# Kernel optimization log

Hardware: AMD Instinct MI355X
Metric: run time of the kernel (lower is better)

## Reference

```python
import jax, jax.numpy as jnp
import numpy as np

B, T_PAST, FUTURE_N = 128, 1024, 512
IN_F, IP, H, OUT_F = 64, 128, 256, 64


def _init(key, shape, fan_in):
    return (jax.random.uniform(key, shape, jnp.float32) * 2.0 - 1.0) / np.sqrt(fan_in).astype(np.float32)


def setup_inputs() -> dict:
    key = jax.random.key(0)
    ks = jax.random.split(key, 16)
    return {
        "x": jax.random.normal(ks[0], (B, T_PAST, IN_F), jnp.float32),
        "future_n": FUTURE_N,
        # encoder: Linear(IN_F -> IP)
        "enc_W": _init(ks[1], (IP, IN_F), IN_F),
        "enc_b": _init(ks[2], (IP,), IN_F),
        # future encoder: Linear(H -> IP)
        "fut_W": _init(ks[3], (IP, H), H),
        "fut_b": _init(ks[4], (IP,), H),
        # decoder: Linear(H -> OUT_F)
        "dec_W": _init(ks[5], (OUT_F, H), H),
        "dec_b": _init(ks[6], (OUT_F,), H),
        # past LSTMCell(IP, H)
        "pW_ih": _init(ks[7], (4 * H, IP), H),
        "pW_hh": _init(ks[8], (4 * H, H), H),
        "pb_ih": _init(ks[9], (4 * H,), H),
        "pb_hh": _init(ks[10], (4 * H,), H),
        # future LSTMCell(IP, H)
        "fW_ih": _init(ks[11], (4 * H, IP), H),
        "fW_hh": _init(ks[12], (4 * H, H), H),
        "fb_ih": _init(ks[13], (4 * H,), H),
        "fb_hh": _init(ks[14], (4 * H,), H),
    }


def _lstm_cell(xt, h, c, W_ih, W_hh, b_ih, b_hh):
    # torch LSTMCell gate order: i, f, g, o
    gates = xt @ W_ih.T + h @ W_hh.T + (b_ih + b_hh)
    i, f, g, o = jnp.split(gates, 4, axis=-1)
    c_new = jax.nn.sigmoid(f) * c + jax.nn.sigmoid(i) * jnp.tanh(g)
    h_new = jax.nn.sigmoid(o) * jnp.tanh(c_new)
    return h_new, c_new


def reference(x, future_n, enc_W, enc_b, fut_W, fut_b, dec_W, dec_b,
              pW_ih, pW_hh, pb_ih, pb_hh, fW_ih, fW_hh, fb_ih, fb_hh):
    batch = x.shape[0]
    hidden = pW_hh.shape[1]
    h0 = jnp.zeros((batch, hidden), x.dtype)
    c0 = jnp.zeros((batch, hidden), x.dtype)

    encoded = x @ enc_W.T + enc_b  # [B, T, IP]

    def past_step(carry, xt):
        h, c = carry
        h, c = _lstm_cell(xt, h, c, pW_ih, pW_hh, pb_ih, pb_hh)
        return (h, c), h

    (h, c), hs_past = jax.lax.scan(past_step, (h0, c0), jnp.swapaxes(encoded, 0, 1))

    def fut_step(carry, _):
        h, c = carry
        inp = h @ fut_W.T + fut_b
        h, c = _lstm_cell(inp, h, c, fW_ih, fW_hh, fb_ih, fb_hh)
        return (h, c), h

    _, hs_fut = jax.lax.scan(fut_step, (h, c), None, length=future_n)

    hs = jnp.concatenate([hs_past, hs_fut], axis=0)  # [T+F, B, H]
    out = jnp.swapaxes(hs, 0, 1) @ dec_W.T + dec_b  # [B, T+F, OUT_F]
    return out
```

## Files before the change

kernel.cpp:

```cpp
#include <hip/hip_runtime.h>

#define B_    128
#define TPAST 1024
#define FN    512
#define TT    1536
#define INF   64
#define IPF   128
#define HD    256
#define NG    1024
#define OUTF  64

typedef _Float16 f16;
typedef _Float16 f16x8 __attribute__((ext_vector_type(8)));
typedef _Float16 f16x4 __attribute__((ext_vector_type(4)));
typedef float    f32x4 __attribute__((ext_vector_type(4)));

template<int N> struct ic { static constexpr int value = N; };

__device__ __forceinline__ float sigm_(float x) {
  return __builtin_amdgcn_rcpf(1.f + __expf(-x));
}
__device__ __forceinline__ float tanh_(float x) {
  return 1.f - 2.f * __builtin_amdgcn_rcpf(1.f + __expf(2.f * x));
}
__device__ __forceinline__ f16x8 oload16(const f16* p) {
  f16x8 v;
  asm volatile("global_load_dwordx4 %0, %1, off\n\ts_waitcnt vmcnt(0)"
               : "=v"(v) : "v"(p));
  return v;
}

extern "C" __global__ void eprep(
    const float* __restrict__ enc_W, const float* __restrict__ enc_b,
    const float* __restrict__ fut_W, const float* __restrict__ fut_b,
    const float* __restrict__ dec_W,
    const float* __restrict__ pW_ih, const float* __restrict__ pW_hh,
    const float* __restrict__ pb_ih, const float* __restrict__ pb_hh,
    const float* __restrict__ fW_ih, const float* __restrict__ fW_hh,
    const float* __restrict__ fb_ih, const float* __restrict__ fb_hh,
    f16* __restrict__ Wp_in, float* __restrict__ bp,
    f16* __restrict__ Wp16, f16* __restrict__ Wf16,
    float* __restrict__ bf, f16* __restrict__ dW16)
{
  int stride = gridDim.x * blockDim.x;
  int gid = blockIdx.x * blockDim.x + threadIdx.x;
  for (int i = gid; i < NG * HD; i += stride) {
    int n = i >> 8, j = i & 255;
    float s = fW_hh[i];
    for (int m = 0; m < IPF; ++m) s += fW_ih[n * IPF + m] * fut_W[m * HD + j];
    Wf16[i] = (f16)s;
    Wp16[i] = (f16)pW_hh[i];
  }
  for (int i = gid; i < NG * INF; i += stride) {
    int n = i >> 6, k = i & 63;
    float s = 0.f;
    for (int m = 0; m < IPF; ++m) s += pW_ih[n * IPF + m] * enc_W[m * INF + k];
    Wp_in[i] = (f16)s;
  }
  for (int i = gid; i < OUTF * HD; i += stride) dW16[i] = (f16)dec_W[i];
  for (int n = gid; n < NG; n += stride) {
    float s1 = pb_ih[n] + pb_hh[n], s2 = fb_ih[n] + fb_hh[n];
    for (int m = 0; m < IPF; ++m) {
      s1 += pW_ih[n * IPF + m] * enc_b[m];
      s2 += fW_ih[n * IPF + m] * fut_b[m];
    }
    bp[n] = s1; bf[n] = s2;
  }
}

extern "C" __global__ __launch_bounds__(64) void epgemm(
    const float* __restrict__ x, const f16* __restrict__ Wp_in,
    const float* __restrict__ bp, f16* __restrict__ P, int t0, int Tc)
{
  int wg = blockIdx.x;
  int tl = wg >> 3, bt = wg & 7;
  int t = t0 + tl;
  int l = (int)threadIdx.x, r = l & 15, g = l >> 4;
  const float* xb = x + ((size_t)(bt * 16 + r) * TPAST + t) * INF;
  f16x8 a[2];
#pragma unroll
  for (int kk = 0; kk < 2; ++kk) {
    const float* px = xb + kk * 32 + g * 8;
    f32x4 v0 = *(const f32x4*)px;
    f32x4 v1 = *(const f32x4*)(px + 4);
#pragma unroll
    for (int e = 0; e < 4; ++e) { a[kk][e] = (f16)v0[e]; a[kk][4 + e] = (f16)v1[e]; }
  }
  for (int nt = 0; nt < 64; ++nt) {
    int n = nt * 16 + r;
    f16x8 b0 = *(const f16x8*)(Wp_in + (size_t)n * INF + g * 8);
    f16x8 b1 = *(const f16x8*)(Wp_in + (size_t)n * INF + 32 + g * 8);
    f32x4 acc = {0.f, 0.f, 0.f, 0.f};
    acc = __builtin_amdgcn_mfma_f32_16x16x32_f16(a[0], b0, acc, 0, 0, 0);
    acc = __builtin_amdgcn_mfma_f32_16x16x32_f16(a[1], b1, acc, 0, 0, 0);
    float bias = bp[n];
    f16x4 hv;
#pragma unroll
    for (int e = 0; e < 4; ++e) hv[e] = (f16)(acc[e] + bias);
    int jh = (n >> 7) & 1;
    int nl = (n >> 8) * 128 + (n & 127);
    f16* Pt = P + (((size_t)(jh * 8 + bt) * Tc + tl) * 512 + nl) * 16;
    *(f16x4*)(Pt + 4 * g) = hv;
  }
}

extern "C" __global__ __launch_bounds__(256, 1)
void erecur(
    const f16* __restrict__ W, const f16* __restrict__ P, int pstep,
    const float* __restrict__ bias,
    f16* __restrict__ hs, f16* __restrict__ h_state, float* __restrict__ c_state,
    f16* __restrict__ Hx, unsigned int* __restrict__ flags,
    int Tc, int seq0, int init_state)
{
  __shared__ f16  Wl[512 * 96];
  __shared__ f16  hb[2][16 * HD];
  __shared__ float cb[128 * 20];
  __shared__ f16  bl[512];

  int tid = (int)threadIdx.x;
  int w = tid >> 6, l = tid & 63, r = l & 15, g = l >> 4;
  int wg = blockIdx.x;
  int bs = wg & 7, jh = wg >> 3;
  int b0 = bs * 16;
  int pwg = wg ^ 8;

  for (int nl = tid; nl < 512; nl += 256) {
    int n_glob = (nl >> 7) * 256 + jh * 128 + (nl & 127);
#pragma unroll
    for (int c8 = 0; c8 < 12; ++c8) {
      f16x8 v = *(const f16x8*)(W + (size_t)n_glob * HD + 160 + c8 * 8);
      *(f16x8*)&Wl[(nl * 96 + c8 * 8) ^ ((nl & 7) << 3)] = v;
    }
  }
  if (bias) {
    for (int i = tid; i < 512; i += 256) {
      int n_glob = (i >> 7) * 256 + jh * 128 + (i & 127);
      bl[i] = (f16)bias[n_glob];
    }
  }
  f16x8 wf[4][2][5];
#pragma unroll
  for (int ga = 0; ga < 4; ++ga)
#pragma unroll
    for (int s = 0; s < 2; ++s) {
      int n_glob = ga * 256 + jh * 128 + w * 32 + s * 16 + r;
#pragma unroll
      for (int kt = 0; kt < 5; ++kt)
        wf[ga][s][kt] = oload16(W + (size_t)n_glob * HD + kt * 32 + g * 8);
    }
  int cur0 = seq0 & 1;
  if (init_state) {
    for (int i = tid; i < 16 * HD; i += 256) hb[cur0][i ^ (((i >> 8) & 7) << 3)] = (f16)0.f;
    for (int i = tid; i < 128 * 20; i += 256) cb[i] = 0.f;
  } else {
    for (int i = tid; i < 16 * HD; i += 256) {
      int b = i >> 8, j = i & 255;
      hb[cur0][i ^ ((b & 7) << 3)] = h_state[(size_t)(b0 + b) * HD + j];
    }
    for (int i = tid; i < 16 * 128; i += 256) {
      int b = i >> 7, j = i & 127;
      cb[j * 20 + b] = c_state[(size_t)(b0 + b) * HD + jh * 128 + j];
    }
  }
  __syncthreads();

  const f16* Pw = P ? (P + (size_t)wg * Tc * pstep) : nullptr;

  for (int tl = 0; tl < Tc; ++tl) {
    int v = seq0 + tl;
    const f16* hbc = hb[v & 1];

    f16x4 pv[4][2];
    if (P) {
#pragma unroll
      for (int ga = 0; ga < 4; ++ga)
#pragma unroll
        for (int s = 0; s < 2; ++s) {
          int nl = ga * 128 + w * 32 + s * 16 + r;
          pv[ga][s] = *(const f16x4*)(Pw + nl * 16 + 4 * g);
        }
    }
    f32x4 acc[4][2];
#pragma unroll
    for (int ga = 0; ga < 4; ++ga)
#pragma unroll
      for (int s = 0; s < 2; ++s) acc[ga][s] = f32x4{0.f, 0.f, 0.f, 0.f};

    auto gemm_kt = [&](auto ktc) {
      constexpr int KT = decltype(ktc)::value;
      f16x8 a = *(const f16x8*)&hbc[(r * HD + KT * 32 + g * 8) ^ ((r & 7) << 3)];
#pragma unroll
      for (int ga = 0; ga < 4; ++ga)
#pragma unroll
        for (int s = 0; s < 2; ++s) {
          if constexpr (KT < 5) {
            acc[ga][s] = __builtin_amdgcn_mfma_f32_16x16x32_f16(a, wf[ga][s][KT], acc[ga][s], 0, 0, 0);
          } else {
            int nl = ga * 128 + w * 32 + s * 16 + r;
            f16x8 bw = *(const f16x8*)&Wl[(nl * 96 + (KT - 5) * 32 + g * 8) ^ ((nl & 7) << 3)];
            acc[ga][s] = __builtin_amdgcn_mfma_f32_16x16x32_f16(a, bw, acc[ga][s], 0, 0, 0);
          }
        }
    };

    if (jh == 0) { gemm_kt(ic<0>{}); gemm_kt(ic<1>{}); gemm_kt(ic<2>{}); gemm_kt(ic<3>{}); }
    else         { gemm_kt(ic<4>{}); gemm_kt(ic<5>{}); gemm_kt(ic<6>{}); gemm_kt(ic<7>{}); }

    if (tl > 0) {
      unsigned tgt = (unsigned)v;
      while (__hip_atomic_load(&flags[pwg], __ATOMIC_ACQUIRE,
                               __HIP_MEMORY_SCOPE_AGENT) < tgt)
        __builtin_amdgcn_s_sleep(1);
      const f16* HxR = Hx + ((size_t)(v & 1) * 16 + pwg) * 2048;
      f16* hbw = hb[v & 1];
#pragma unroll
      for (int u0 = 0; u0 < 2; ++u0) {
        int u = tid + u0 * 256;
        int j = u >> 2, q = u & 3;
        union { unsigned long long u64; f16 h4[4]; } pk;
        pk.u64 = __hip_atomic_load((const unsigned long long*)(HxR + j * 16 + q * 4),
                                   __ATOMIC_RELAXED, __HIP_MEMORY_SCOPE_AGENT);
        int jg = (jh ^ 1) * 128 + j;
#pragma unroll
        for (int e = 0; e < 4; ++e) {
          int b = q * 4 + e;
          hbw[(b * HD + jg) ^ ((b & 7) << 3)] = pk.h4[e];
        }
      }
      __syncthreads();
    }

    if (jh == 0) { gemm_kt(ic<4>{}); gemm_kt(ic<5>{}); gemm_kt(ic<6>{}); gemm_kt(ic<7>{}); }
    else         { gemm_kt(ic<0>{}); gemm_kt(ic<1>{}); gemm_kt(ic<2>{}); gemm_kt(ic<3>{}); }

    f16* hbn = hb[(v + 1) & 1];
    f16* HxW = Hx + ((size_t)((v + 1) & 1) * 16 + wg) * 2048;
    f16 hsave[2][4];
#pragma unroll
    for (int s = 0; s < 2; ++s) {
      int j = w * 32 + s * 16 + r;
      int jg = jh * 128 + j;
      f32x4 cold = *(f32x4*)&cb[j * 20 + 4 * g];
      float gadd[4];
#pragma unroll
      for (int ga = 0; ga < 4; ++ga)
        gadd[ga] = P ? 0.f : (float)bl[ga * 128 + j];
      f32x4 cnew;
      union { unsigned long long u; f16 h4[4]; } pk;
#pragma unroll
      for (int e = 0; e < 4; ++e) {
        float xi = acc[0][s][e] + gadd[0];
        float xf = acc[1][s][e] + gadd[1];
        float xg = acc[2][s][e] + gadd[2];
        float xo = acc[3][s][e] + gadd[3];
        if (P) {
          xi += (float)pv[0][s][e]; xf += (float)pv[1][s][e];
          xg += (float)pv[2][s][e]; xo += (float)pv[3][s][e];
        }
        float ii = sigm_(xi), ff = sigm_(xf), oo = sigm_(xo), gg = tanh_(xg);
        float cn = ff * cold[e] + ii * gg;
        cnew[e] = cn;
        pk.h4[e] = (f16)(oo * tanh_(cn));
        hsave[s][e] = pk.h4[e];
      }
      *(f32x4*)&cb[j * 20 + 4 * g] = cnew;
      __hip_atomic_store((unsigned long long*)(HxW + j * 16 + 4 * g), pk.u,
                         __ATOMIC_RELAXED, __HIP_MEMORY_SCOPE_AGENT);
#pragma unroll
      for (int e = 0; e < 4; ++e) {
        int b = 4 * g + e;
        hbn[(b * HD + jg) ^ ((b & 7) << 3)] = pk.h4[e];
      }
    }
    __syncthreads();

    if (tid == 0)
      __hip_atomic_store(&flags[wg], (unsigned)(v + 1),
                         __ATOMIC_RELEASE, __HIP_MEMORY_SCOPE_AGENT);

#pragma unroll
    for (int s = 0; s < 2; ++s) {
      int jg = jh * 128 + w * 32 + s * 16 + r;
#pragma unroll
      for (int e = 0; e < 4; ++e)
        hs[((size_t)tl * B_ + b0 + 4 * g + e) * HD + jg] = hsave[s][e];
    }
    if (P) Pw += pstep;
  }
  const f16* hbf = hb[(seq0 + Tc) & 1];
  for (int i = tid; i < 16 * 128; i += 256) {
    int b = i >> 7, j = i & 127;
    int jg = jh * 128 + j;
    h_state[(size_t)(b0 + b) * HD + jg] = hbf[(b * HD + jg) ^ ((b & 7) << 3)];
    c_state[(size_t)(b0 + b) * HD + jg] = cb[j * 20 + b];
  }
}

extern "C" __global__ __launch_bounds__(64) void edec(
    const f16* __restrict__ hs, const f16* __restrict__ dW,
    const float* __restrict__ dec_b, float* __restrict__ out, int t0, int Tc)
{
  int wg = blockIdx.x;
  int tt = wg >> 7, b = wg & 127;
  int l = (int)threadIdx.x, r = l & 15, g = l >> 4;
  f16x8 wfr[4][8];
#pragma unroll
  for (int nt = 0; nt < 4; ++nt)
#pragma unroll
    for (int kt = 0; kt < 8; ++kt)
      wfr[nt][kt] = *(const f16x8*)(dW + (size_t)(nt * 16 + r) * HD + kt * 32 + g * 8);
  float bb[4];
#pragma unroll
  for (int nt = 0; nt < 4; ++nt) bb[nt] = dec_b[nt * 16 + r];
  f32x4 acc[2][4];
  const f32x4 zero4 = {0.f, 0.f, 0.f, 0.f};
#pragma unroll
  for (int mt = 0; mt < 2; ++mt)
#pragma unroll
    for (int nt = 0; nt < 4; ++nt) acc[mt][nt] = zero4;
#pragma unroll
  for (int mt = 0; mt < 2; ++mt)
#pragma unroll
    for (int kt = 0; kt < 8; ++kt) {
      f16x8 a = *(const f16x8*)(hs + ((size_t)(tt * 32 + mt * 16 + r) * B_ + b) * HD + kt * 32 + g * 8);
#pragma unroll
      for (int nt = 0; nt < 4; ++nt)
        acc[mt][nt] = __builtin_amdgcn_mfma_f32_16x16x32_f16(a, wfr[nt][kt], acc[mt][nt], 0, 0, 0);
    }
#pragma unroll
  for (int mt = 0; mt < 2; ++mt)
#pragma unroll
    for (int nt = 0; nt < 4; ++nt)
#pragma unroll
      for (int e = 0; e < 4; ++e) {
        int t = t0 + tt * 32 + mt * 16 + 4 * g + e;
        out[((size_t)b * TT + t) * OUTF + nt * 16 + r] = acc[mt][nt][e] + bb[nt];
      }
}

extern "C" void kernel_launch(void* const* d_in, const int* in_sizes, int n_in,
                              void* d_out, int out_size, void* d_ws, size_t ws_size,
                              hipStream_t stream)
{
  const float* x     = (const float*)d_in[0];
  const float* enc_W = (const float*)d_in[2];
  const float* enc_b = (const float*)d_in[3];
  const float* fut_W = (const float*)d_in[4];
  const float* fut_b = (const float*)d_in[5];
  const float* dec_W = (const float*)d_in[6];
  const float* dec_b = (const float*)d_in[7];
  const float* pW_ih = (const float*)d_in[8];
  const float* pW_hh = (const float*)d_in[9];
  const float* pb_ih = (const float*)d_in[10];
  const float* pb_hh = (const float*)d_in[11];
  const float* fW_ih = (const float*)d_in[12];
  const float* fW_hh = (const float*)d_in[13];
  const float* fb_ih = (const float*)d_in[14];
  const float* fb_hh = (const float*)d_in[15];
  (void)in_sizes; (void)n_in; (void)out_size;

  char* p = (char*)d_ws;
  auto alloc = [&](size_t bytes) { char* q = p; p += (bytes + 255) & ~(size_t)255; return q; };
  f16*   Wp_in = (f16*)  alloc((size_t)NG * INF * 2);
  float* bp    = (float*)alloc((size_t)NG * 4);
  f16*   Wp16  = (f16*)  alloc((size_t)NG * HD * 2);
  f16*   Wf16  = (f16*)  alloc((size_t)NG * HD * 2);
  float* bfb   = (float*)alloc((size_t)NG * 4);
  f16*   dW16  = (f16*)  alloc((size_t)OUTF * HD * 2);
  f16*   h_st  = (f16*)  alloc((size_t)B_ * HD * 2);
  float* c_st  = (float*)alloc((size_t)B_ * HD * 4);
  f16*   Hx    = (f16*)  alloc((size_t)2 * 16 * 2048 * 2);
  unsigned int* flags = (unsigned int*)alloc(64);
  size_t fixed = (size_t)(p - (char*)d_ws);

  auto need = [&](int rr) {
    size_t pp = (size_t)(rr < TPAST ? rr : TPAST) * NG * B_ * 2;
    size_t hh = (size_t)rr * B_ * HD * 2;
    return pp + hh + 4096;
  };
  size_t avail = ws_size > fixed ? ws_size - fixed : 0;
  int R = 128;
  if (avail >= need(1536)) R = 1536;
  else if (avail >= need(512)) R = 512;
  else if (avail >= need(256)) R = 256;

  f16* Pbuf = (f16*)alloc((size_t)(R < TPAST ? R : TPAST) * NG * B_ * 2);
  f16* HS   = (f16*)alloc((size_t)R * B_ * HD * 2);

  hipMemsetAsync(flags, 0, 64, stream);

  eprep<<<512, 256, 0, stream>>>(enc_W, enc_b, fut_W, fut_b, dec_W,
                                 pW_ih, pW_hh, pb_ih, pb_hh,
                                 fW_ih, fW_hh, fb_ih, fb_hh,
                                 Wp_in, bp, Wp16, Wf16, bfb, dW16);

  for (int t0 = 0; t0 < TPAST; t0 += R) {
    int Tc = (TPAST - t0) < R ? (TPAST - t0) : R;
    epgemm<<<Tc * 8, 64, 0, stream>>>(x, Wp_in, bp, Pbuf, t0, Tc);
    erecur<<<16, 256, 0, stream>>>(Wp16, Pbuf, 512 * 16, nullptr, HS, h_st, c_st,
                                   Hx, flags, Tc, t0, t0 == 0 ? 1 : 0);
    edec<<<(Tc / 32) * B_, 64, 0, stream>>>(HS, dW16, dec_b, (float*)d_out, t0, Tc);
  }
  for (int t0 = TPAST; t0 < TT; t0 += R) {
    int Tc = (TT - t0) < R ? (TT - t0) : R;
    erecur<<<16, 256, 0, stream>>>(Wf16, nullptr, 0, bfb, HS, h_st, c_st,
                                   Hx, flags, Tc, t0, 0);
    edec<<<(Tc / 32) * B_, 64, 0, stream>>>(HS, dW16, dec_b, (float*)d_out, t0, Tc);
  }
}
```

Baseline: 6.443 ms.

## Transpose recurrent MFMA operands, read partner h directly into registers, prefetch P

Swaps the MFMA operand order so the weights are the A operand and h is the B operand, which transposes the output layout to batch-in-lanes. The partner half of h is now loaded straight from the exchange buffer into register fragments instead of being scattered into LDS, so one __syncthreads per step goes away and the LDS h buffer shrinks to the local half. The precomputed input projection P gets a new layout and is double-buffered in registers one step ahead. The hs and h_state stores become vectorized 16-byte writes from LDS. The cost is more live registers and more indexing complexity in the cell update.

```diff
diff --git a/kernel.cpp b/kernel.cpp
--- a/kernel.cpp
+++ b/kernel.cpp
@@ -88,19 +88,19 @@
   }
   for (int nt = 0; nt < 64; ++nt) {
     int n = nt * 16 + r;
-    f16x8 b0 = *(const f16x8*)(Wp_in + (size_t)n * INF + g * 8);
-    f16x8 b1 = *(const f16x8*)(Wp_in + (size_t)n * INF + 32 + g * 8);
+    f16x8 w0 = *(const f16x8*)(Wp_in + (size_t)n * INF + g * 8);
+    f16x8 w1 = *(const f16x8*)(Wp_in + (size_t)n * INF + 32 + g * 8);
     f32x4 acc = {0.f, 0.f, 0.f, 0.f};
-    acc = __builtin_amdgcn_mfma_f32_16x16x32_f16(a[0], b0, acc, 0, 0, 0);
-    acc = __builtin_amdgcn_mfma_f32_16x16x32_f16(a[1], b1, acc, 0, 0, 0);
-    float bias = bp[n];
+    acc = __builtin_amdgcn_mfma_f32_16x16x32_f16(w0, a[0], acc, 0, 0, 0);
+    acc = __builtin_amdgcn_mfma_f32_16x16x32_f16(w1, a[1], acc, 0, 0, 0);
+    f32x4 bias4 = *(const f32x4*)&bp[nt * 16 + 4 * g];
     f16x4 hv;
 #pragma unroll
-    for (int e = 0; e < 4; ++e) hv[e] = (f16)(acc[e] + bias);
-    int jh = (n >> 7) & 1;
-    int nl = (n >> 8) * 128 + (n & 127);
-    f16* Pt = P + (((size_t)(jh * 8 + bt) * Tc + tl) * 512 + nl) * 16;
-    *(f16x4*)(Pt + 4 * g) = hv;
+    for (int e = 0; e < 4; ++e) hv[e] = (f16)(acc[e] + bias4[e]);
+    int ga = nt >> 4, jhp = (nt >> 3) & 1;
+    int nl = ga * 128 + (nt & 7) * 16 + 4 * g;
+    f16* Pt = P + (((size_t)(jhp * 8 + bt) * Tc + tl) * 16 + r) * 512;
+    *(f16x4*)(Pt + nl) = hv;
   }
 }
 
@@ -113,7 +113,7 @@
     int Tc, int seq0, int init_state)
 {
   __shared__ f16  Wl[512 * 96];
-  __shared__ f16  hb[2][16 * HD];
+  __shared__ f16  hb[2][16 * 128];
   __shared__ float cb[128 * 20];
   __shared__ f16  bl[512];
 
@@ -125,17 +125,17 @@
   int pwg = wg ^ 8;
 
   for (int nl = tid; nl < 512; nl += 256) {
-    int n_glob = (nl >> 7) * 256 + jh * 128 + (nl & 127);
+    int ng = (nl >> 7) * 256 + jh * 128 + (nl & 127);
 #pragma unroll
     for (int c8 = 0; c8 < 12; ++c8) {
-      f16x8 v = *(const f16x8*)(W + (size_t)n_glob * HD + 160 + c8 * 8);
+      f16x8 v = *(const f16x8*)(W + (size_t)ng * HD + 160 + c8 * 8);
       *(f16x8*)&Wl[(nl * 96 + c8 * 8) ^ ((nl & 7) << 3)] = v;
     }
   }
   if (bias) {
     for (int i = tid; i < 512; i += 256) {
-      int n_glob = (i >> 7) * 256 + jh * 128 + (i & 127);
-      bl[i] = (f16)bias[n_glob];
+      int ng = (i >> 7) * 256 + jh * 128 + (i & 127);
+      bl[i] = (f16)bias[ng];
     }
   }
   f16x8 wf[4][2][5];
@@ -143,134 +143,140 @@
   for (int ga = 0; ga < 4; ++ga)
 #pragma unroll
     for (int s = 0; s < 2; ++s) {
-      int n_glob = ga * 256 + jh * 128 + w * 32 + s * 16 + r;
+      int ng = ga * 256 + jh * 128 + w * 32 + s * 16 + r;
 #pragma unroll
       for (int kt = 0; kt < 5; ++kt)
-        wf[ga][s][kt] = oload16(W + (size_t)n_glob * HD + kt * 32 + g * 8);
+        wf[ga][s][kt] = oload16(W + (size_t)ng * HD + kt * 32 + g * 8);
     }
   int cur0 = seq0 & 1;
+  f16x8 pa[4];
   if (init_state) {
-    for (int i = tid; i < 16 * HD; i += 256) hb[cur0][i ^ (((i >> 8) & 7) << 3)] = (f16)0.f;
+    for (int i = tid; i < 16 * 128; i += 256) {
+      int b = i >> 7, jl = i & 127;
+      hb[cur0][(b * 128 + jl) ^ ((b & 7) << 3)] = (f16)0.f;
+    }
     for (int i = tid; i < 128 * 20; i += 256) cb[i] = 0.f;
+    f16x8 z = {};
+#pragma unroll
+    for (int kt = 0; kt < 4; ++kt) pa[kt] = z;
   } else {
-    for (int i = tid; i < 16 * HD; i += 256) {
-      int b = i >> 8, j = i & 255;
-      hb[cur0][i ^ ((b & 7) << 3)] = h_state[(size_t)(b0 + b) * HD + j];
-    }
     for (int i = tid; i < 16 * 128; i += 256) {
-      int b = i >> 7, j = i & 127;
-      cb[j * 20 + b] = c_state[(size_t)(b0 + b) * HD + jh * 128 + j];
-    }
+      int b = i >> 7, jl = i & 127;
+      hb[cur0][(b * 128 + jl) ^ ((b & 7) << 3)] =
+          h_state[(size_t)(b0 + b) * HD + jh * 128 + jl];
+    }
+    for (int i = tid; i < 16 * 128; i += 256) {
+      int b = i >> 7, jl = i & 127;
+      cb[jl * 20 + b] = c_state[(size_t)(b0 + b) * HD + jh * 128 + jl];
+    }
+#pragma unroll
+    for (int kt = 0; kt < 4; ++kt)
+      pa[kt] = *(const f16x8*)(h_state + (size_t)(b0 + r) * HD + (jh ^ 1) * 128 + kt * 32 + g * 8);
+  }
+  const f16* Pw = P ? (P + (size_t)wg * Tc * pstep) : nullptr;
+  f16x4 pvA[4][2], pvB[4][2];
+  if (P) {
+#pragma unroll
+    for (int ga = 0; ga < 4; ++ga)
+#pragma unroll
+      for (int s = 0; s < 2; ++s)
+        pvA[ga][s] = *(const f16x4*)(Pw + r * 512 + ga * 128 + w * 32 + s * 16 + 4 * g);
   }
   __syncthreads();
-
-  const f16* Pw = P ? (P + (size_t)wg * Tc * pstep) : nullptr;
 
   for (int tl = 0; tl < Tc; ++tl) {
     int v = seq0 + tl;
     const f16* hbc = hb[v & 1];
 
-    f16x4 pv[4][2];
-    if (P) {
-#pragma unroll
-      for (int ga = 0; ga < 4; ++ga)
-#pragma unroll
-        for (int s = 0; s < 2; ++s) {
-          int nl = ga * 128 + w * 32 + s * 16 + r;
-          pv[ga][s] = *(const f16x4*)(Pw + nl * 16 + 4 * g);
-        }
-    }
     f32x4 acc[4][2];
 #pragma unroll
     for (int ga = 0; ga < 4; ++ga)
 #pragma unroll
       for (int s = 0; s < 2; ++s) acc[ga][s] = f32x4{0.f, 0.f, 0.f, 0.f};
 
-    auto gemm_kt = [&](auto ktc) {
+    auto do_kt = [&](auto ktc, f16x8 hfrag) {
       constexpr int KT = decltype(ktc)::value;
-      f16x8 a = *(const f16x8*)&hbc[(r * HD + KT * 32 + g * 8) ^ ((r & 7) << 3)];
 #pragma unroll
       for (int ga = 0; ga < 4; ++ga)
 #pragma unroll
         for (int s = 0; s < 2; ++s) {
           if constexpr (KT < 5) {
-            acc[ga][s] = __builtin_amdgcn_mfma_f32_16x16x32_f16(a, wf[ga][s][KT], acc[ga][s], 0, 0, 0);
+            acc[ga][s] = __builtin_amdgcn_mfma_f32_16x16x32_f16(wf[ga][s][KT], hfrag, acc[ga][s], 0, 0, 0);
           } else {
             int nl = ga * 128 + w * 32 + s * 16 + r;
-            f16x8 bw = *(const f16x8*)&Wl[(nl * 96 + (KT - 5) * 32 + g * 8) ^ ((nl & 7) << 3)];
-            acc[ga][s] = __builtin_amdgcn_mfma_f32_16x16x32_f16(a, bw, acc[ga][s], 0, 0, 0);
+            f16x8 aw = *(const f16x8*)&Wl[(nl * 96 + (KT - 5) * 32 + g * 8) ^ ((nl & 7) << 3)];
+            acc[ga][s] = __builtin_amdgcn_mfma_f32_16x16x32_f16(aw, hfrag, acc[ga][s], 0, 0, 0);
           }
         }
     };
-
-    if (jh == 0) { gemm_kt(ic<0>{}); gemm_kt(ic<1>{}); gemm_kt(ic<2>{}); gemm_kt(ic<3>{}); }
-    else         { gemm_kt(ic<4>{}); gemm_kt(ic<5>{}); gemm_kt(ic<6>{}); gemm_kt(ic<7>{}); }
+    auto ownfrag = [&](int ktl) {
+      return *(const f16x8*)&hbc[(r * 128 + ktl * 32 + g * 8) ^ ((r & 7) << 3)];
+    };
+
+    if (jh == 0) {
+      do_kt(ic<0>{}, ownfrag(0)); do_kt(ic<1>{}, ownfrag(1));
+      do_kt(ic<2>{}, ownfrag(2)); do_kt(ic<3>{}, ownfrag(3));
+    } else {
+      do_kt(ic<4>{}, ownfrag(0)); do_kt(ic<5>{}, ownfrag(1));
+      do_kt(ic<6>{}, ownfrag(2)); do_kt(ic<7>{}, ownfrag(3));
+    }
 
     if (tl > 0) {
-      unsigned tgt = (unsigned)v;
       while (__hip_atomic_load(&flags[pwg], __ATOMIC_ACQUIRE,
-                               __HIP_MEMORY_SCOPE_AGENT) < tgt)
+                               __HIP_MEMORY_SCOPE_AGENT) < (unsigned)v)
         __builtin_amdgcn_s_sleep(1);
       const f16* HxR = Hx + ((size_t)(v & 1) * 16 + pwg) * 2048;
-      f16* hbw = hb[v & 1];
-#pragma unroll
-      for (int u0 = 0; u0 < 2; ++u0) {
-        int u = tid + u0 * 256;
-        int j = u >> 2, q = u & 3;
-        union { unsigned long long u64; f16 h4[4]; } pk;
-        pk.u64 = __hip_atomic_load((const unsigned long long*)(HxR + j * 16 + q * 4),
-                                   __ATOMIC_RELAXED, __HIP_MEMORY_SCOPE_AGENT);
-        int jg = (jh ^ 1) * 128 + j;
-#pragma unroll
-        for (int e = 0; e < 4; ++e) {
-          int b = q * 4 + e;
-          hbw[(b * HD + jg) ^ ((b & 7) << 3)] = pk.h4[e];
-        }
-      }
-      __syncthreads();
-    }
-
-    if (jh == 0) { gemm_kt(ic<4>{}); gemm_kt(ic<5>{}); gemm_kt(ic<6>{}); gemm_kt(ic<7>{}); }
-    else         { gemm_kt(ic<0>{}); gemm_kt(ic<1>{}); gemm_kt(ic<2>{}); gemm_kt(ic<3>{}); }
+#pragma unroll
+      for (int kt = 0; kt < 4; ++kt)
+        pa[kt] = *(const f16x8*)(HxR + r * 128 + kt * 32 + g * 8);
+    }
+    if (P && tl + 1 < Tc) {
+#pragma unroll
+      for (int ga = 0; ga < 4; ++ga)
+#pragma unroll
+        for (int s = 0; s < 2; ++s)
+          pvB[ga][s] = *(const f16x4*)(Pw + pstep + r * 512 + ga * 128 + w * 32 + s * 16 + 4 * g);
+    }
+    if (jh == 0) {
+      do_kt(ic<4>{}, pa[0]); do_kt(ic<5>{}, pa[1]);
+      do_kt(ic<6>{}, pa[2]); do_kt(ic<7>{}, pa[3]);
+    } else {
+      do_kt(ic<0>{}, pa[0]); do_kt(ic<1>{}, pa[1]);
+      do_kt(ic<2>{}, pa[2]); do_kt(ic<3>{}, pa[3]);
+    }
 
     f16* hbn = hb[(v + 1) & 1];
     f16* HxW = Hx + ((size_t)((v + 1) & 1) * 16 + wg) * 2048;
-    f16 hsave[2][4];
 #pragma unroll
     for (int s = 0; s < 2; ++s) {
-      int j = w * 32 + s * 16 + r;
-      int jg = jh * 128 + j;
-      f32x4 cold = *(f32x4*)&cb[j * 20 + 4 * g];
-      float gadd[4];
-#pragma unroll
-      for (int ga = 0; ga < 4; ++ga)
-        gadd[ga] = P ? 0.f : (float)bl[ga * 128 + j];
-      f32x4 cnew;
+      int j4 = w * 32 + s * 16 + 4 * g;
+      float cold[4];
+#pragma unroll
+      for (int e = 0; e < 4; ++e) cold[e] = cb[(j4 + e) * 20 + r];
+      f16x4 b4[4];
+      if (!P) {
+#pragma unroll
+        for (int ga = 0; ga < 4; ++ga) b4[ga] = *(const f16x4*)&bl[ga * 128 + j4];
+      }
       union { unsigned long long u; f16 h4[4]; } pk;
 #pragma unroll
       for (int e = 0; e < 4; ++e) {
-        float xi = acc[0][s][e] + gadd[0];
-        float xf = acc[1][s][e] + gadd[1];
-        float xg = acc[2][s][e] + gadd[2];
-        float xo = acc[3][s][e] + gadd[3];
+        float xi = acc[0][s][e], xf = acc[1][s][e], xg = acc[2][s][e], xo = acc[3][s][e];
         if (P) {
-          xi += (float)pv[0][s][e]; xf += (float)pv[1][s][e];
-          xg += (float)pv[2][s][e]; xo += (float)pv[3][s][e];
+          xi += (float)pvA[0][s][e]; xf += (float)pvA[1][s][e];
+          xg += (float)pvA[2][s][e]; xo += (float)pvA[3][s][e];
+        } else {
+          xi += (float)b4[0][e]; xf += (float)b4[1][e];
+          xg += (float)b4[2][e]; xo += (float)b4[3][e];
         }
         float ii = sigm_(xi), ff = sigm_(xf), oo = sigm_(xo), gg = tanh_(xg);
         float cn = ff * cold[e] + ii * gg;
-        cnew[e] = cn;
+        cb[(j4 + e) * 20 + r] = cn;
         pk.h4[e] = (f16)(oo * tanh_(cn));
-        hsave[s][e] = pk.h4[e];
       }
-      *(f32x4*)&cb[j * 20 + 4 * g] = cnew;
-      __hip_atomic_store((unsigned long long*)(HxW + j * 16 + 4 * g), pk.u,
+      __hip_atomic_store((unsigned long long*)(HxW + r * 128 + j4), pk.u,
                          __ATOMIC_RELAXED, __HIP_MEMORY_SCOPE_AGENT);
-#pragma unroll
-      for (int e = 0; e < 4; ++e) {
-        int b = 4 * g + e;
-        hbn[(b * HD + jg) ^ ((b & 7) << 3)] = pk.h4[e];
-      }
+      *(unsigned long long*)&hbn[(r * 128 + j4) ^ ((r & 7) << 3)] = pk.u;
     }
     __syncthreads();
 
@@ -278,21 +284,28 @@
       __hip_atomic_store(&flags[wg], (unsigned)(v + 1),
                          __ATOMIC_RELEASE, __HIP_MEMORY_SCOPE_AGENT);
 
-#pragma unroll
-    for (int s = 0; s < 2; ++s) {
-      int jg = jh * 128 + w * 32 + s * 16 + r;
-#pragma unroll
-      for (int e = 0; e < 4; ++e)
-        hs[((size_t)tl * B_ + b0 + 4 * g + e) * HD + jg] = hsave[s][e];
-    }
-    if (P) Pw += pstep;
-  }
-  const f16* hbf = hb[(seq0 + Tc) & 1];
+    {
+      int b = tid >> 4, seg = tid & 15;
+      f16x8 hv = *(const f16x8*)&hbn[(b * 128 + seg * 8) ^ ((b & 7) << 3)];
+      *(f16x8*)(hs + ((size_t)tl * B_ + b0 + b) * HD + jh * 128 + seg * 8) = hv;
+    }
+    if (P) {
+#pragma unroll
+      for (int ga = 0; ga < 4; ++ga)
+#pragma unroll
+        for (int s = 0; s < 2; ++s) pvA[ga][s] = pvB[ga][s];
+      Pw += pstep;
+    }
+  }
+  {
+    const f16* hbf = hb[(seq0 + Tc) & 1];
+    int b = tid >> 4, seg = tid & 15;
+    f16x8 hv = *(const f16x8*)&hbf[(b * 128 + seg * 8) ^ ((b & 7) << 3)];
+    *(f16x8*)(h_state + (size_t)(b0 + b) * HD + jh * 128 + seg * 8) = hv;
+  }
   for (int i = tid; i < 16 * 128; i += 256) {
-    int b = i >> 7, j = i & 127;
-    int jg = jh * 128 + j;
-    h_state[(size_t)(b0 + b) * HD + jg] = hbf[(b * HD + jg) ^ ((b & 7) << 3)];
-    c_state[(size_t)(b0 + b) * HD + jg] = cb[j * 20 + b];
+    int b = i >> 7, jl = i & 127;
+    c_state[(size_t)(b0 + b) * HD + jh * 128 + jl] = cb[jl * 20 + b];
   }
 }
 
```

New measurement: 6.783 ms. 1.05x slower.
